# Optimization experiments

Measured on AMD Instinct MI355X. Metric: run time of the kernel, lower is better.

Reference implementation:

```python
import jax, jax.numpy as jnp
import numpy as np

N = 30000      # nodes
IN = 768       # input feature dim
C = 128        # hidden channels (= conv out_dim, = gate dim)
HEADS = 4      # attention heads (TransformerConv and Semantic)
DH = 128       # per-head dim (concat=False -> out_channels)
R = 3          # num relations
E = 80000      # edges per relation
NEG = 0.01     # LeakyReLU slope


def setup_inputs() -> dict:
    key = jax.random.key(0)
    ks = iter(jax.random.split(key, 64))
    def nx(shape):
        return jax.random.normal(next(ks), shape, dtype=jnp.float32) * 0.02
    inp = {}
    inp["x"] = jax.random.normal(next(ks), (N, IN), dtype=jnp.float32)
    inp["edges"] = jax.random.randint(next(ks), (R, 2, E), 0, N, dtype=jnp.int32)
    inp["lin1_W"] = nx((IN, C)); inp["lin1_b"] = jnp.zeros((C,), jnp.float32)
    for l in ("l1", "l2"):
        inp[f"{l}_Wq"] = nx((R, C, HEADS * DH)); inp[f"{l}_bq"] = jnp.zeros((R, HEADS * DH), jnp.float32)
        inp[f"{l}_Wk"] = nx((R, C, HEADS * DH)); inp[f"{l}_bk"] = jnp.zeros((R, HEADS * DH), jnp.float32)
        inp[f"{l}_Wv"] = nx((R, C, HEADS * DH)); inp[f"{l}_bv"] = jnp.zeros((R, HEADS * DH), jnp.float32)
        inp[f"{l}_Ws"] = nx((R, C, DH));         inp[f"{l}_bs"] = jnp.zeros((R, DH), jnp.float32)
        inp[f"{l}_gW"] = nx((C + DH, C));        inp[f"{l}_gb"] = jnp.zeros((C,), jnp.float32)
        inp[f"{l}_sW1"] = nx((HEADS, C, C));     inp[f"{l}_sb1"] = jnp.zeros((HEADS, C), jnp.float32)
        inp[f"{l}_sw2"] = nx((HEADS, C))
    inp["lin2_W"] = nx((C, C)); inp["lin2_b"] = jnp.zeros((C,), jnp.float32)
    inp["clf_W"] = nx((C, 2)); inp["clf_b"] = jnp.zeros((2,), jnp.float32)
    return inp


def lrelu(x):
    return jnp.where(x >= 0, x, NEG * x)


def transformer_conv(x, src, dst, Wq, bq, Wk, bk, Wv, bv, Ws, bs):
    # PyG TransformerConv, heads=HEADS, concat=False (head mean), root_weight=True, eval (no dropout)
    n = x.shape[0]
    q = (x @ Wq + bq).reshape(n, HEADS, DH)
    k = (x @ Wk + bk).reshape(n, HEADS, DH)
    v = (x @ Wv + bv).reshape(n, HEADS, DH)
    logits = (q[dst] * k[src]).sum(-1) / np.sqrt(DH)      # [E, H]
    m = jax.ops.segment_max(logits, dst, num_segments=n)  # scatter-softmax (stable)
    a = jnp.exp(logits - m[dst])
    s = jax.ops.segment_sum(a, dst, num_segments=n)
    alpha = a / s[dst]
    agg = jax.ops.segment_sum(alpha[:, :, None] * v[src], dst, num_segments=n)  # [N, H, DH]
    return agg.mean(axis=1) + x @ Ws + bs


def semantic(Hm, sW1, sb1, sw2):
    # Hm: [N, R, C]; per-head scoring MLP -> softmax over relations -> weighted sum, averaged over heads
    t = jnp.tanh(jnp.einsum('nrc,hco->hnro', Hm, sW1) + sb1[:, None, None, :])  # [H, N, R, C]
    scores = jnp.einsum('hnro,ho->hnr', t, sw2).mean(axis=1)                    # [H, R]
    beta = jax.nn.softmax(scores, axis=-1)
    return jnp.einsum('hr,nrc->nc', beta, Hm) / HEADS


def rgt_layer(x, edges, Wq, bq, Wk, bk, Wv, bv, Ws, bs, gW, gb, sW1, sb1, sw2):
    Hs = []
    for r in range(R):  # small fixed relation loop
        src, dst = edges[r, 0], edges[r, 1]
        U = transformer_conv(x, src, dst, Wq[r], bq[r], Wk[r], bk[r], Wv[r], bv[r], Ws[r], bs[r])
        Z = jax.nn.sigmoid(jnp.concatenate([U, x], axis=1) @ gW + gb)
        Hs.append(jnp.tanh(U) * Z + x * (1.0 - Z))
    Hm = jnp.stack(Hs, axis=1)  # [N, R, C]
    return semantic(Hm, sW1, sb1, sw2)


def reference(x, edges, lin1_W, lin1_b,
              l1_Wq, l1_bq, l1_Wk, l1_bk, l1_Wv, l1_bv, l1_Ws, l1_bs, l1_gW, l1_gb, l1_sW1, l1_sb1, l1_sw2,
              l2_Wq, l2_bq, l2_Wk, l2_bk, l2_Wv, l2_bv, l2_Ws, l2_bs, l2_gW, l2_gb, l2_sW1, l2_sb1, l2_sw2,
              lin2_W, lin2_b, clf_W, clf_b):
    h = lrelu(x @ lin1_W + lin1_b)
    h = rgt_layer(h, edges, l1_Wq, l1_bq, l1_Wk, l1_bk, l1_Wv, l1_bv, l1_Ws, l1_bs, l1_gW, l1_gb, l1_sW1, l1_sb1, l1_sw2)
    h = rgt_layer(h, edges, l2_Wq, l2_bq, l2_Wk, l2_bk, l2_Wv, l2_bv, l2_Ws, l2_bs, l2_gW, l2_gb, l2_sW1, l2_sb1, l2_sw2)
    h = lrelu(h @ lin2_W + lin2_b)
    return h @ clf_W + clf_b
```

## Files before the change

kernel.cpp:

```cpp
#include <hip/hip_runtime.h>
#include <math.h>

#define Nn 30000
#define RR 3
#define EE 80000
#define MT_M 235

#define SAP 72
#define EP_LD 68
#define KBIG 0x40000000

typedef __attribute__((ext_vector_type(8))) short bf16x8;
typedef __attribute__((ext_vector_type(4))) float f32x4;

__device__ __forceinline__ unsigned short f2bf(float f) {
    union { float f; unsigned u; } v; v.f = f;
    unsigned r = v.u + 0x7fff + ((v.u >> 16) & 1);
    return (unsigned short)(r >> 16);
}
__device__ __forceinline__ float fast_tanh(float x) {
    float e = __expf(2.f * x);
    return 1.f - 2.f / (e + 1.f);
}
__device__ __forceinline__ void unpack8(uint4 u, float* f) {
    union { unsigned u; float f; } a;
    a.u = u.x << 16;          f[0] = a.f;
    a.u = u.x & 0xffff0000u;  f[1] = a.f;
    a.u = u.y << 16;          f[2] = a.f;
    a.u = u.y & 0xffff0000u;  f[3] = a.f;
    a.u = u.z << 16;          f[4] = a.f;
    a.u = u.z & 0xffff0000u;  f[5] = a.f;
    a.u = u.w << 16;          f[6] = a.f;
    a.u = u.w & 0xffff0000u;  f[7] = a.f;
}

__device__ __forceinline__ void mfma_core(
    const short* __restrict__ A, int lda,
    const short* __restrict__ A2, int lda2, int ksplit,
    const short* __restrict__ Bt,
    int M, int K, int m0, int n0,
    short* As, short* Bs, f32x4 (&acc)[4][4])
{
    const int t = threadIdx.x;
    const int srow = t >> 3;
    const int scol = (t & 7) << 3;
    const int lane = t & 63;
    const int wave = t >> 6;
    const int wm = (wave >> 1) << 6;
    const int wn = (wave & 1) << 6;
    const int fr = lane & 15;
    const int quad = lane >> 4;
// ... 70 lines not shown
                ws[(quad * 4 + reg) * EP_LD + ni * 16 + fr] = acc[mi][ni][reg];
        int gr = m0 + wm + mi * 16 + rrow;
        if (gr >= M) continue;
        int gc = n0 + wn + cseg;
        float vals[16];
        #pragma unroll
        for (int j = 0; j < 16; j++) {
            float v = ws[rrow * EP_LD + cseg + j] + bias[gc + j];
            if (act == 1) v = (v >= 0.f) ? v : 0.01f * v;
            vals[j] = v;
        }
        if (C) {
            float* cp = C + (size_t)gr * ldc + gc;
            #pragma unroll
            for (int j4 = 0; j4 < 4; j4++)
                *(float4*)(cp + j4 * 4) = make_float4(vals[j4 * 4], vals[j4 * 4 + 1],
                                                      vals[j4 * 4 + 2], vals[j4 * 4 + 3]);
        }
        if (Cbf) {
            unsigned pk[8];
            #pragma unroll
            for (int j2 = 0; j2 < 8; j2++)
                pk[j2] = ((unsigned)f2bf(vals[2 * j2 + 1]) << 16) | (unsigned)f2bf(vals[2 * j2]);
            unsigned* bp = (unsigned*)(Cbf + (size_t)gr * ldcbf + gc);
            *(uint4*)bp       = make_uint4(pk[0], pk[1], pk[2], pk[3]);
            *(uint4*)(bp + 4) = make_uint4(pk[4], pk[5], pk[6], pk[7]);
        }
    }
}

__global__ __launch_bounds__(256) void gemm_qkvs_v4(
    const short* __restrict__ A,
    const short* __restrict__ Wt, const float* __restrict__ bias,
    short* __restrict__ qhat3, short* __restrict__ Ubf, int M)
{
    __shared__ short As[128 * SAP];
    __shared__ short Bs[128 * SAP];
    f32x4 acc[4][4];
    #pragma unroll
    for (int i = 0; i < 4; i++)
        #pragma unroll
        for (int j = 0; j < 4; j++) acc[i][j] = (f32x4){0.f, 0.f, 0.f, 0.f};
    int m0 = blockIdx.y * 128, bx = blockIdx.x, n0 = bx * 128;
    mfma_core(A, 128, A, 128, KBIG, Wt, M, 128, m0, n0, As, Bs, acc);

    const int t = threadIdx.x;
    const int lane = t & 63, wave = t >> 6;
    const int wm = (wave >> 1) << 6, wn = (wave & 1) << 6;
    const int fr = lane & 15, quad = lane >> 4;
    float* ws = (float*)As + wave * 16 * EP_LD;
    const int rrow = lane >> 2;
    const int cseg = (lane & 3) << 4;
    #pragma unroll
    for (int mi = 0; mi < 4; mi++) {
        #pragma unroll
        for (int ni = 0; ni < 4; ni++)
            #pragma unroll
            for (int reg = 0; reg < 4; reg++)
                ws[(quad * 4 + reg) * EP_LD + ni * 16 + fr] = acc[mi][ni][reg];
        int gr = m0 + wm + mi * 16 + rrow;
        if (gr >= M) continue;
        int lc = wn + cseg;
        float vals[16];
        #pragma unroll
        for (int j = 0; j < 16; j++)
            vals[j] = ws[rrow * EP_LD + cseg + j] + bias[n0 + lc + j];
        unsigned pk[8];
        #pragma unroll
        for (int j2 = 0; j2 < 8; j2++)
            pk[j2] = ((unsigned)f2bf(vals[2 * j2 + 1]) << 16) | (unsigned)f2bf(vals[2 * j2]);
        short* dst;
        if (bx < 12) {
            int r = bx >> 2;
            dst = qhat3 + ((size_t)(r * Nn + gr)) * 512 + (bx - r * 4) * 128 + lc;
        } else {
            dst = Ubf + (size_t)gr * 384 + (bx - 12) * 128 + lc;
        }
        unsigned* bp = (unsigned*)dst;
        *(uint4*)bp       = make_uint4(pk[0], pk[1], pk[2], pk[3]);
        *(uint4*)(bp + 4) = make_uint4(pk[4], pk[5], pk[6], pk[7]);
    }
}

__global__ __launch_bounds__(256) void attn_v4(
    const short* __restrict__ qhat3, const short* __restrict__ hbf,
    const int* __restrict__ rowptr3, const int* __restrict__ col3,
    short* __restrict__ Ah3)
{
    int wid = ((blockIdx.x * blockDim.x + threadIdx.x) >> 6);
    int lane = threadIdx.x & 63;
    if (wid >= 3 * Nn) return;
    int r = wid / Nn, n = wid - r * Nn;
    const int* rowptr = rowptr3 + r * (Nn + 1);
    const int* colb = col3 + r * EE;
    int beg = rowptr[n], end = rowptr[n + 1];

    uint4 qv = ((const uint4*)(qhat3 + ((size_t)r * Nn + n) * 512))[lane];
    float qf[8];
    unpack8(qv, qf);
    const int l16 = lane & 15;

    float m = -INFINITY, s = 0.f;
    float acc[8] = {0.f, 0.f, 0.f, 0.f, 0.f, 0.f, 0.f, 0.f};

    for (int i = beg; i < end; i++) {
        int src = colb[i];
        uint4 hv = ((const uint4*)(hbf + (size_t)src * 128))[l16];
        float hf[8];
        unpack8(hv, hf);
        float p = qf[0] * hf[0] + qf[1] * hf[1] + qf[2] * hf[2] + qf[3] * hf[3]
                + qf[4] * hf[4] + qf[5] * hf[5] + qf[6] * hf[6] + qf[7] * hf[7];
        p += __shfl_xor(p, 1);
        p += __shfl_xor(p, 2);
        p += __shfl_xor(p, 4);
        p += __shfl_xor(p, 8);
        float nm = fmaxf(m, p);
        float sc = __expf(m - nm);
        float pe = __expf(p - nm);
        s = s * sc + pe;
        #pragma unroll
        for (int j = 0; j < 8; j++) acc[j] = acc[j] * sc + pe * hf[j];
        m = nm;
    }

    float inv = (s > 0.f) ? 1.f / s : 0.f;
    #pragma unroll
    for (int j = 0; j < 8; j++) acc[j] *= inv;

    unsigned p0 = ((unsigned)f2bf(acc[1]) << 16) | (unsigned)f2bf(acc[0]);
    unsigned p1 = ((unsigned)f2bf(acc[3]) << 16) | (unsigned)f2bf(acc[2]);
    unsigned p2 = ((unsigned)f2bf(acc[5]) << 16) | (unsigned)f2bf(acc[4]);
    unsigned p3 = ((unsigned)f2bf(acc[7]) << 16) | (unsigned)f2bf(acc[6]);
    *(uint4*)(Ah3 + ((size_t)r * Nn + n) * 512 + lane * 8) = make_uint4(p0, p1, p2, p3);
}

__global__ __launch_bounds__(256) void ufin_mfma(
    const short* __restrict__ Ah3, const short* __restrict__ wvst,
    const float* __restrict__ bvmean, const int* __restrict__ rowptr3,
    short* __restrict__ U_bf, int M)
{
    __shared__ short As[128 * SAP];
    __shared__ short Bs[128 * SAP];
    f32x4 acc[4][4];
    #pragma unroll
    for (int i = 0; i < 4; i++)
        #pragma unroll
        for (int j = 0; j < 4; j++) acc[i][j] = (f32x4){0.f, 0.f, 0.f, 0.f};
    int r = blockIdx.z;
    int m0 = blockIdx.y * 128;
    const short* Ar = Ah3 + (size_t)r * Nn * 512;
    mfma_core(Ar, 512, Ar, 512, KBIG, wvst + r * 65536, M, 512, m0, 0, As, Bs, acc);

    const int t = threadIdx.x;
    const int lane = t & 63, wave = t >> 6;
    const int wm = (wave >> 1) << 6, wn = (wave & 1) << 6;
    const int fr = lane & 15, quad = lane >> 4;
    float* ws = (float*)As + wave * 16 * EP_LD;
    const int rrow = lane >> 2;
    const int cseg = (lane & 3) << 4;
    #pragma unroll
    for (int mi = 0; mi < 4; mi++) {
        #pragma unroll
        for (int ni = 0; ni < 4; ni++)
            #pragma unroll
            for (int reg = 0; reg < 4; reg++)
                ws[(quad * 4 + reg) * EP_LD + ni * 16 + fr] = acc[mi][ni][reg];
        int gr = m0 + wm + mi * 16 + rrow;
        if (gr >= M) continue;
        int gc = wn + cseg;
        int be = rowptr3[r * (Nn + 1) + gr];
        int en = rowptr3[r * (Nn + 1) + gr + 1];
        float mk = (en > be) ? 1.f : 0.f;
        short* up = U_bf + (size_t)gr * 384 + r * 128 + gc;
        uint4 u0 = *(const uint4*)up;
        uint4 u1 = *(const uint4*)(up + 8);
        float uv[16];
        unpack8(u0, uv); unpack8(u1, uv + 8);
        float vals[16];
        #pragma unroll
        for (int j = 0; j < 16; j++)
            vals[j] = ws[rrow * EP_LD + cseg + j] + uv[j] + mk * bvmean[r * 128 + gc + j];
        unsigned pk[8];
        #pragma unroll
        for (int j2 = 0; j2 < 8; j2++)
            pk[j2] = ((unsigned)f2bf(vals[2 * j2 + 1]) << 16) | (unsigned)f2bf(vals[2 * j2]);
        unsigned* bp = (unsigned*)up;
        *(uint4*)bp       = make_uint4(pk[0], pk[1], pk[2], pk[3]);
        *(uint4*)(bp + 4) = make_uint4(pk[4], pk[5], pk[6], pk[7]);
    }
}

__global__ __launch_bounds__(256) void gate_mfma(
    const short* __restrict__ Ubf,
    const short* __restrict__ Hbf,
    const short* __restrict__ gWt, const float* __restrict__ gb,
    const float* __restrict__ Hf,
    float* __restrict__ Hm, short* __restrict__ HmBf,
    int M)
{
    __shared__ short As[128 * SAP];
    __shared__ short Bs[128 * SAP];
    f32x4 acc[4][4];
    #pragma unroll
    for (int i = 0; i < 4; i++)
        #pragma unroll
        for (int j = 0; j < 4; j++) acc[i][j] = (f32x4){0.f, 0.f, 0.f, 0.f};
    int r = blockIdx.z;
    int m0 = blockIdx.y * 128;
    mfma_core(Ubf + r * 128, 384, Hbf, 128, 128, gWt, M, 256, m0, 0, As, Bs, acc);

    const int t = threadIdx.x;
    const int lane = t & 63, wave = t >> 6;
    const int wm = (wave >> 1) << 6, wn = (wave & 1) << 6;
    const int fr = lane & 15, quad = lane >> 4;
    float* ws = (float*)As + wave * 16 * EP_LD;
    const int rrow = lane >> 2;
    const int cseg = (lane & 3) << 4;
    #pragma unroll
    for (int mi = 0; mi < 4; mi++) {
        #pragma unroll
        for (int ni = 0; ni < 4; ni++)
            #pragma unroll
            for (int reg = 0; reg < 4; reg++)
                ws[(quad * 4 + reg) * EP_LD + ni * 16 + fr] = acc[mi][ni][reg];
        int gr = m0 + wm + mi * 16 + rrow;
        if (gr >= M) continue;
        int gc = wn + cseg;
        const short* up = Ubf + (size_t)gr * 384 + r * 128 + gc;
        const float* hp = Hf + (size_t)gr * 128 + gc;
        float uv[16], hv[16];
        uint4 u0 = *(const uint4*)up;
        uint4 u1 = *(const uint4*)(up + 8);
        unpack8(u0, uv); unpack8(u1, uv + 8);
        #pragma unroll
        for (int j4 = 0; j4 < 4; j4++)
            *(float4*)(hv + j4 * 4) = *(const float4*)(hp + j4 * 4);
        float vals[16];
        #pragma unroll
        for (int j = 0; j < 16; j++) {
            float g = ws[rrow * EP_LD + cseg + j] + gb[gc + j];
            float z = 1.f / (1.f + __expf(-g));
            vals[j] = fast_tanh(uv[j]) * z + hv[j] * (1.f - z);
        }
        float* cp = Hm + (size_t)gr * 384 + r * 128 + gc;
        #pragma unroll
        for (int j4 = 0; j4 < 4; j4++)
            *(float4*)(cp + j4 * 4) = make_float4(vals[j4 * 4], vals[j4 * 4 + 1],
                                                  vals[j4 * 4 + 2], vals[j4 * 4 + 3]);
        unsigned pk[8];
        #pragma unroll
        for (int j2 = 0; j2 < 8; j2++)
            pk[j2] = ((unsigned)f2bf(vals[2 * j2 + 1]) << 16) | (unsigned)f2bf(vals[2 * j2]);
        unsigned* bp = (unsigned*)(HmBf + (size_t)gr * 384 + r * 128 + gc);
        *(uint4*)bp       = make_uint4(pk[0], pk[1], pk[2], pk[3]);
        *(uint4*)(bp + 4) = make_uint4(pk[4], pk[5], pk[6], pk[7]);
    }
}

__global__ __launch_bounds__(256) void semantic_mfma(
    const short* __restrict__ HmBf, const short* __restrict__ sW1t,
    const float* __restrict__ sb1, const float* __restrict__ sw2,
    float* __restrict__ partial, int M)
{
    __shared__ short As[128 * SAP];
    __shared__ short Bs[128 * SAP];
    __shared__ float red4[4];
    f32x4 acc[4][4];
    #pragma unroll
    for (int i = 0; i < 4; i++)
        #pragma unroll
        for (int j = 0; j < 4; j++) acc[i][j] = (f32x4){0.f, 0.f, 0.f, 0.f};
    int head = blockIdx.x, r = blockIdx.z;
    int m0 = blockIdx.y * 128, n0 = head * 128;
    mfma_core(HmBf + r * 128, 384, HmBf + r * 128, 384, KBIG, sW1t, M, 128, m0, n0, As, Bs, acc);
    const int t = threadIdx.x;
    const int lane = t & 63, wave = t >> 6;
    const int wm = (wave >> 1) << 6, wn = (wave & 1) << 6;
    const int fr = lane & 15, quad = lane >> 4;
    float local = 0.f;
    #pragma unroll
    for (int ni = 0; ni < 4; ni++) {
        int gc = n0 + wn + ni * 16 + fr;
        float b = sb1[gc], w2 = sw2[gc];
        #pragma unroll
        for (int mi = 0; mi < 4; mi++) {
            #pragma unroll
            for (int reg = 0; reg < 4; reg++) {
                int gr = m0 + wm + mi * 16 + quad * 4 + reg;
// ... 53 lines not shown
    float w0 = w[0], w1 = w[1], w2 = w[2];
    float4 v = make_float4(w0 * a.x + w1 * b.x + w2 * c.x,
                           w0 * a.y + w1 * b.y + w2 * c.y,
                           w0 * a.z + w1 * b.z + w2 * c.z,
                           w0 * a.w + w1 * b.w + w2 * c.w);
    *(float4*)(h + (size_t)n * 128 + c4) = v;
    unsigned p0 = ((unsigned)f2bf(v.y) << 16) | (unsigned)f2bf(v.x);
    unsigned p1 = ((unsigned)f2bf(v.w) << 16) | (unsigned)f2bf(v.z);
    *(uint2*)(hbf + (size_t)n * 128 + c4) = make_uint2(p0, p1);
}

__global__ void convert_bf16_kernel(const float* __restrict__ src, unsigned* __restrict__ dst, int n_pairs)
{
    int i = blockIdx.x * blockDim.x + threadIdx.x;
    if (i >= n_pairs) return;
    float2 f = ((const float2*)src)[i];
    dst[i] = ((unsigned)f2bf(f.y) << 16) | (unsigned)f2bf(f.x);
}

__global__ void prep_global_kernel(const float* __restrict__ lin1_W, const float* __restrict__ lin2_W,
                                   short* __restrict__ lin1Wt, short* __restrict__ lin2Wt)
{
    int id = blockIdx.x * blockDim.x + threadIdx.x;
    if (id < 98304) {
        int n = id / 768, k = id % 768;
        lin1Wt[id] = (short)f2bf(lin1_W[k * 128 + n]);
    } else if (id < 114688) {
        int r = id - 98304;
        int n = r / 128, k = r % 128;
        lin2Wt[r] = (short)f2bf(lin2_W[k * 128 + n]);
    }
}

__global__ void prep_layer_v4(
    const float* __restrict__ Ws, const float* __restrict__ bs,
    const float* __restrict__ gW, const float* __restrict__ sW1,
    const float* __restrict__ Wv, const float* __restrict__ bv,
    short* __restrict__ Wt4, short* __restrict__ gWt,
    short* __restrict__ sW1t, short* __restrict__ wvst,
    float* __restrict__ B4, float* __restrict__ bvmean)
{
    const int S0 = 49152;
    const int S1 = S0 + 32768;
    const int S2 = S1 + 65536;
    const int S3 = S2 + 196608;
    const int S4 = S3 + 384;
    const int S5 = S4 + 384;
    int id = blockIdx.x * blockDim.x + threadIdx.x;
    if (id < S0) {
        int n = id / 128, k = id - n * 128;
        int r = n >> 7, c = n & 127;
        Wt4[(size_t)(1536 + n) * 128 + k] = (short)f2bf(Ws[(size_t)r * 16384 + k * 128 + c]);
    } else if (id < S1) {
        int q = id - S0;
        int n = q / 256, k = q - n * 256;
        gWt[q] = (short)f2bf(gW[k * 128 + n]);
    } else if (id < S2) {
        int q = id - S1;
        int h = q / 16384, rem = q - h * 16384;
        int n = rem / 128, k = rem - n * 128;
        sW1t[q] = (short)f2bf(sW1[(size_t)h * 16384 + k * 128 + n]);
    } else if (id < S3) {
        int q = id - S2;
        int r = q / 65536, rem = q - r * 65536;
        int d = rem / 512, mcol = rem - d * 512;
        int hh = mcol >> 7, j = mcol & 127;
        wvst[q] = (short)f2bf(0.25f * Wv[(size_t)r * 65536 + j * 512 + hh * 128 + d]);
    } else if (id < S4) {
        int q = id - S3;
        B4[1536 + q] = bs[q];
    } else if (id < S5) {
        int q = id - S4;
        int r = q >> 7, d = q & 127;
        bvmean[q] = 0.25f * (bv[r * 512 + d] + bv[r * 512 + 128 + d]
                           + bv[r * 512 + 256 + d] + bv[r * 512 + 384 + d]);
    }
}

__global__ __launch_bounds__(256) void gmat_v2(
    const float* __restrict__ Wq0, const float* __restrict__ Wk0, const float* __restrict__ bq0,
    const float* __restrict__ Wq1, const float* __restrict__ Wk1, const float* __restrict__ bq1,
    short* __restrict__ Wt4, float* __restrict__ B4)
{
    __shared__ float WqL[128 * 129];
    __shared__ float WkL[16 * 128];
    const int jg = blockIdx.x;
    const int h  = blockIdx.y;
    const int lz = blockIdx.z;
    const int l = lz / 3, r = lz - l * 3;
    const float* Wq = l ? Wq1 : Wq0;
    const float* Wk = l ? Wk1 : Wk0;
    const float* bq = l ? bq1 : bq0;
    short* Wt = Wt4 + (size_t)l * 245760;
    float* Bb = B4 + l * 1920;
    const float scale = 0.088388347648318447f;
    const int t = threadIdx.x;

    for (int v = t; v < 4096; v += 256) {
        int i = v >> 5, d4 = (v & 31) << 2;
        float4 q = *(const float4*)(Wq + (size_t)r * 65536 + i * 512 + h * 128 + d4);
        float* wp = WqL + i * 129 + d4;
        wp[0] = q.x; wp[1] = q.y; wp[2] = q.z; wp[3] = q.w;
    }
    for (int v = t; v < 512; v += 256) {
        int jl = v >> 5, d4 = (v & 31) << 2;
        float4 q = *(const float4*)(Wk + (size_t)r * 65536 + (jg * 16 + jl) * 512 + h * 128 + d4);
        float* wp = WkL + jl * 128 + d4;
        wp[0] = q.x; wp[1] = q.y; wp[2] = q.z; wp[3] = q.w;
    }
    __syncthreads();

    const int i = t & 127;
    const int jh = t >> 7;
    const float* wk = WkL + jh * 8 * 128;
    float acc[8] = {0.f, 0.f, 0.f, 0.f, 0.f, 0.f, 0.f, 0.f};
    #pragma unroll 4
    for (int d = 0; d < 128; d++) {
        float wq = WqL[i * 129 + d];
        #pragma unroll
        for (int jj = 0; jj < 8; jj++)
            acc[jj] += wq * wk[jj * 128 + d];
    }
    short* wrow = Wt + ((size_t)(r * 512 + h * 128 + jg * 16 + jh * 8)) * 128 + i;
    #pragma unroll
    for (int jj = 0; jj < 8; jj++)
        wrow[(size_t)jj * 128] = (short)f2bf(scale * acc[jj]);

// ... 71 lines not shown
    if (n >= M) return;
    const float* row = t + (size_t)n * 128;
    float a0 = b[0], a1 = b[1];
    #pragma unroll
    for (int kk = 0; kk < 128; kk++) {
        float a = row[kk];
        a0 += a * W[kk * 2];
        a1 += a * W[kk * 2 + 1];
    }
    out[n * 2] = a0;
    out[n * 2 + 1] = a1;
}

extern "C" void kernel_launch(void* const* d_in, const int* in_sizes, int n_in,
                              void* d_out, int out_size, void* d_ws, size_t ws_size,
                              hipStream_t stream)
{
    const float* x      = (const float*)d_in[0];
    const int*   edges  = (const int*)d_in[1];
    const float* lin1_W = (const float*)d_in[2];
    const float* lin1_b = (const float*)d_in[3];
    const int L0 = 4, L1 = 17;
    const float* lin2_W = (const float*)d_in[30];
    const float* lin2_b = (const float*)d_in[31];
    const float* clf_W  = (const float*)d_in[32];
    const float* clf_b  = (const float*)d_in[33];
    float* out = (float*)d_out;

    char* w = (char*)d_ws;
    size_t off = 0;
    auto alloc = [&](size_t bytes) { void* p = w + off; off = (off + bytes + 255) & ~(size_t)255; return p; };
    float* h      = (float*)alloc((size_t)Nn * 128 * 4);
    short* h_bf   = (short*)alloc((size_t)Nn * 128 * 2);
    short* U_bf   = (short*)alloc((size_t)Nn * 384 * 2);
    const size_t QH = (size_t)3 * Nn * 512 * 2;
    char* BIG     = (char*)alloc(2 * QH);
    short* qhat3  = (short*)BIG;
    short* Ah3    = (short*)(BIG + QH);
    short* x_bf   = (short*)BIG;
    float* Hm     = (float*)BIG;
    short* Hm_bf  = (short*)(BIG + (size_t)Nn * 384 * 4);
    float* lin2o  = (float*)BIG;
    short* lin1Wt = (short*)alloc((size_t)98304 * 2);
    short* lin2Wt = (short*)alloc((size_t)16384 * 2);
    short* qkvsWt4 = (short*)alloc((size_t)2 * 245760 * 2);
    short* gWt    = (short*)alloc((size_t)2 * 32768 * 2);
    short* sW1t   = (short*)alloc((size_t)2 * 65536 * 2);
    short* wvst   = (short*)alloc((size_t)2 * 196608 * 2);
    float* qkvsB4 = (float*)alloc((size_t)2 * 1920 * 4);
    float* bvmean = (float*)alloc((size_t)2 * 384 * 4);
    int* rowptr3  = (int*)alloc((size_t)3 * (Nn + 1) * 4);
    int* cnt3     = (int*)alloc((size_t)3 * Nn * 4);
    int* col3     = (int*)alloc((size_t)3 * EE * 4);
    float* partial = (float*)alloc((size_t)12 * MT_M * 4);
    float* scores = (float*)alloc(12 * 4);
    float* wmix   = (float*)alloc(3 * 4);

    const int MT = MT_M;
    dim3 blk(256);

    {
        int n_pairs = Nn * 768 / 2;
        convert_bf16_kernel<<<(n_pairs + 255) / 256, blk, 0, stream>>>(x, (unsigned*)x_bf, n_pairs);
        prep_global_kernel<<<(114688 + 255) / 256, blk, 0, stream>>>(lin1_W, lin2_W, lin1Wt, lin2Wt);
        for (int l = 0; l < 2; l++) {
            int base = (l == 0) ? L0 : L1;
            prep_layer_v4<<<(344832 + 255) / 256, blk, 0, stream>>>(
                (const float*)d_in[base + 6], (const float*)d_in[base + 7],
                (const float*)d_in[base + 8], (const float*)d_in[base + 10],
                (const float*)d_in[base + 4], (const float*)d_in[base + 5],
                qkvsWt4 + (size_t)l * 245760, gWt + (size_t)l * 32768,
                sW1t + (size_t)l * 65536, wvst + (size_t)l * 196608,
                qkvsB4 + (size_t)l * 1920, bvmean + (size_t)l * 384);
        }
        gmat_v2<<<dim3(8, 4, 6), blk, 0, stream>>>(
            (const float*)d_in[L0 + 0], (const float*)d_in[L0 + 2], (const float*)d_in[L0 + 1],
            (const float*)d_in[L1 + 0], (const float*)d_in[L1 + 2], (const float*)d_in[L1 + 1],
            qkvsWt4, qkvsB4);
        zero_i32_kernel<<<(3 * Nn + 255) / 256, blk, 0, stream>>>(cnt3, 3 * Nn);
        hist3_kernel<<<(3 * EE + 255) / 256, blk, 0, stream>>>(edges, cnt3);
        scan3_kernel<<<3, 1024, 0, stream>>>(cnt3, rowptr3);
        zero_i32_kernel<<<(3 * Nn + 255) / 256, blk, 0, stream>>>(cnt3, 3 * Nn);
        scatter3_kernel<<<(3 * EE + 255) / 256, blk, 0, stream>>>(edges, rowptr3, cnt3, col3);
    }

    gemm_mfma<<<dim3(1, MT), blk, 0, stream>>>(
        x_bf, 768, x_bf, 768, KBIG, lin1Wt, lin1_b, h, 128, h_bf, 128, Nn, 768, 1);

    for (int l = 0; l < 2; l++) {
        int base = (l == 0) ? L0 : L1;
        const float* gb  = (const float*)d_in[base + 9];
        const float* sb1 = (const float*)d_in[base + 11];
        const float* sw2 = (const float*)d_in[base + 12];
        short* lWt4   = qkvsWt4 + (size_t)l * 245760;
        short* lgWt   = gWt + (size_t)l * 32768;
        short* lsW1t  = sW1t + (size_t)l * 65536;
        short* lwvst  = wvst + (size_t)l * 196608;
        float* lB4    = qkvsB4 + (size_t)l * 1920;
        float* lbvm   = bvmean + (size_t)l * 384;

        gemm_qkvs_v4<<<dim3(15, MT), blk, 0, stream>>>(
            h_bf, lWt4, lB4, qhat3, U_bf, Nn);

        attn_v4<<<(3 * Nn + 3) / 4, blk, 0, stream>>>(qhat3, h_bf, rowptr3, col3, Ah3);

        ufin_mfma<<<dim3(1, MT, 3), blk, 0, stream>>>(Ah3, lwvst, lbvm, rowptr3, U_bf, Nn);

        gate_mfma<<<dim3(1, MT, 3), blk, 0, stream>>>(
            U_bf, h_bf, lgWt, gb, h, Hm, Hm_bf, Nn);

        semantic_mfma<<<dim3(4, MT, 3), blk, 0, stream>>>(Hm_bf, lsW1t, sb1, sw2, partial, Nn);
        reduce12_kernel<<<12, 64, 0, stream>>>(partial, scores);
        compute_w_kernel<<<1, 64, 0, stream>>>(scores, wmix, 1.f / (float)Nn);
        mix_kernel<<<(Nn * 32 + 255) / 256, blk, 0, stream>>>(Hm, wmix, h, h_bf, Nn * 32);
    }

    gemm_mfma<<<dim3(1, MT), blk, 0, stream>>>(
        h_bf, 128, h_bf, 128, KBIG, lin2Wt, lin2_b, lin2o, 128, (short*)nullptr, 0, Nn, 128, 1);
    clf_kernel<<<(Nn + 255) / 256, blk, 0, stream>>>(lin2o, clf_W, clf_b, out, Nn);
}
```

Measured before the change: 812.5 us.

## Fuse value projection, skip projection and gate into one MFMA kernel

The root/skip projection (h@Ws) moves out of the QKVS GEMM and into the value-projection GEMM by concatenating K to 640 (Ah3 plus h). The result U stays in LDS as bf16, and the gating GEMM plus sigmoid/tanh blend run in the same kernel. This removes the U_bf round-trip through global memory and one kernel launch per layer. In exchange, the gate GEMM reads B fragments straight from global without LDS staging, and the epilogue writes Hm with scalar per-element stores instead of vectorised ones.

```diff
diff --git a/kernel.cpp b/kernel.cpp
--- a/kernel.cpp
+++ b/kernel.cpp
@@ -8,6 +8,7 @@
 
 #define SAP 72
 #define EP_LD 68
+#define UTS 136
 #define KBIG 0x40000000
 
 typedef __attribute__((ext_vector_type(8))) short bf16x8;
@@ -17,6 +18,11 @@
     union { float f; unsigned u; } v; v.f = f;
     unsigned r = v.u + 0x7fff + ((v.u >> 16) & 1);
     return (unsigned short)(r >> 16);
+}
+__device__ __forceinline__ float bf2f(short h) {
+    union { unsigned u; float f; } v;
+    v.u = ((unsigned)(unsigned short)h) << 16;
+    return v.f;
 }
 __device__ __forceinline__ float fast_tanh(float x) {
     float e = __expf(2.f * x);
@@ -153,7 +159,7 @@
 __global__ __launch_bounds__(256) void gemm_qkvs_v4(
     const short* __restrict__ A,
     const short* __restrict__ Wt, const float* __restrict__ bias,
-    short* __restrict__ qhat3, short* __restrict__ Ubf, int M)
+    short* __restrict__ qhat3, int M)
 {
     __shared__ short As[128 * SAP];
     __shared__ short Bs[128 * SAP];
@@ -172,6 +178,7 @@
     float* ws = (float*)As + wave * 16 * EP_LD;
     const int rrow = lane >> 2;
     const int cseg = (lane & 3) << 4;
+    const int r = bx >> 2;
     #pragma unroll
     for (int mi = 0; mi < 4; mi++) {
         #pragma unroll
@@ -190,14 +197,7 @@
         #pragma unroll
         for (int j2 = 0; j2 < 8; j2++)
             pk[j2] = ((unsigned)f2bf(vals[2 * j2 + 1]) << 16) | (unsigned)f2bf(vals[2 * j2]);
-        short* dst;
-        if (bx < 12) {
-            int r = bx >> 2;
-            dst = qhat3 + ((size_t)(r * Nn + gr)) * 512 + (bx - r * 4) * 128 + lc;
-        } else {
-            dst = Ubf + (size_t)gr * 384 + (bx - 12) * 128 + lc;
-        }
-        unsigned* bp = (unsigned*)dst;
+        unsigned* bp = (unsigned*)(qhat3 + ((size_t)(r * Nn + gr)) * 512 + (bx - r * 4) * 128 + lc);
         *(uint4*)bp       = make_uint4(pk[0], pk[1], pk[2], pk[3]);
         *(uint4*)(bp + 4) = make_uint4(pk[4], pk[5], pk[6], pk[7]);
     }
@@ -255,126 +255,102 @@
     *(uint4*)(Ah3 + ((size_t)r * Nn + n) * 512 + lane * 8) = make_uint4(p0, p1, p2, p3);
 }
 
-__global__ __launch_bounds__(256) void ufin_mfma(
-    const short* __restrict__ Ah3, const short* __restrict__ wvst,
-    const float* __restrict__ bvmean, const int* __restrict__ rowptr3,
-    short* __restrict__ U_bf, int M)
-{
-    __shared__ short As[128 * SAP];
-    __shared__ short Bs[128 * SAP];
+__global__ __launch_bounds__(256) void ugate_mfma(
+    const short* __restrict__ Ah3, const short* __restrict__ w640t,
+    const float* __restrict__ bs, const float* __restrict__ bvmean,
+    const int* __restrict__ rowptr3,
+    const short* __restrict__ gWt, const float* __restrict__ gb,
+    const short* __restrict__ Hbf, const float* __restrict__ Hf,
+    float* __restrict__ Hm, short* __restrict__ HmBf, int M)
+{
+    __shared__ short LDSb[2 * 128 * SAP];
+    short* As = LDSb;
+    short* Bs = LDSb + 128 * SAP;
     f32x4 acc[4][4];
     #pragma unroll
     for (int i = 0; i < 4; i++)
         #pragma unroll
         for (int j = 0; j < 4; j++) acc[i][j] = (f32x4){0.f, 0.f, 0.f, 0.f};
-    int r = blockIdx.z;
-    int m0 = blockIdx.y * 128;
-    const short* Ar = Ah3 + (size_t)r * Nn * 512;
-    mfma_core(Ar, 512, Ar, 512, KBIG, wvst + r * 65536, M, 512, m0, 0, As, Bs, acc);
+    const int r = blockIdx.z;
+    const int m0 = blockIdx.y * 128;
+    mfma_core(Ah3 + (size_t)r * Nn * 512, 512, Hbf, 128, 512,
+              w640t + (size_t)r * 81920, M, 640, m0, 0, As, Bs, acc);
 
     const int t = threadIdx.x;
     const int lane = t & 63, wave = t >> 6;
     const int wm = (wave >> 1) << 6, wn = (wave & 1) << 6;
     const int fr = lane & 15, quad = lane >> 4;
-    float* ws = (float*)As + wave * 16 * EP_LD;
-    const int rrow = lane >> 2;
-    const int cseg = (lane & 3) << 4;
+    short* Ut = LDSb;
+    const int rp = r * (Nn + 1);
+
     #pragma unroll
     for (int mi = 0; mi < 4; mi++) {
         #pragma unroll
+        for (int reg = 0; reg < 4; reg++) {
+            int row = wm + mi * 16 + quad * 4 + reg;
+            int gr = m0 + row;
+            float mk = 0.f;
+            if (gr < M) mk = (rowptr3[rp + gr + 1] > rowptr3[rp + gr]) ? 1.f : 0.f;
+            #pragma unroll
+            for (int ni = 0; ni < 4; ni++) {
+                int col = wn + ni * 16 + fr;
+                float u = acc[mi][ni][reg] + bs[r * 128 + col] + mk * bvmean[r * 128 + col];
+                Ut[row * UTS + col] = (short)f2bf(u);
+            }
+        }
+    }
+    __syncthreads();
+
+    f32x4 gacc[4][4];
+    #pragma unroll
+    for (int i = 0; i < 4; i++)
+        #pragma unroll
+        for (int j = 0; j < 4; j++) gacc[i][j] = (f32x4){0.f, 0.f, 0.f, 0.f};
+    #pragma unroll
+    for (int kc = 0; kc < 8; kc++) {
+        bf16x8 af[4], bfr[4];
+        #pragma unroll
+        for (int mi = 0; mi < 4; mi++) {
+            int row = wm + mi * 16 + fr;
+            if (kc < 4) {
+                af[mi] = *(const bf16x8*)(Ut + row * UTS + kc * 32 + quad * 8);
+            } else {
+                int gr = m0 + row;
+                bf16x8 v = {0, 0, 0, 0, 0, 0, 0, 0};
+                if (gr < M) v = *(const bf16x8*)(Hbf + (size_t)gr * 128 + (kc - 4) * 32 + quad * 8);
+                af[mi] = v;
+            }
+        }
+        #pragma unroll
         for (int ni = 0; ni < 4; ni++)
-            #pragma unroll
-            for (int reg = 0; reg < 4; reg++)
-                ws[(quad * 4 + reg) * EP_LD + ni * 16 + fr] = acc[mi][ni][reg];
-        int gr = m0 + wm + mi * 16 + rrow;
-        if (gr >= M) continue;
-        int gc = wn + cseg;
-        int be = rowptr3[r * (Nn + 1) + gr];
-        int en = rowptr3[r * (Nn + 1) + gr + 1];
-        float mk = (en > be) ? 1.f : 0.f;
-        short* up = U_bf + (size_t)gr * 384 + r * 128 + gc;
-        uint4 u0 = *(const uint4*)up;
-        uint4 u1 = *(const uint4*)(up + 8);
-        float uv[16];
-        unpack8(u0, uv); unpack8(u1, uv + 8);
-        float vals[16];
-        #pragma unroll
-        for (int j = 0; j < 16; j++)
-            vals[j] = ws[rrow * EP_LD + cseg + j] + uv[j] + mk * bvmean[r * 128 + gc + j];
-        unsigned pk[8];
-        #pragma unroll
-        for (int j2 = 0; j2 < 8; j2++)
-            pk[j2] = ((unsigned)f2bf(vals[2 * j2 + 1]) << 16) | (unsigned)f2bf(vals[2 * j2]);
-        unsigned* bp = (unsigned*)up;
-        *(uint4*)bp       = make_uint4(pk[0], pk[1], pk[2], pk[3]);
-        *(uint4*)(bp + 4) = make_uint4(pk[4], pk[5], pk[6], pk[7]);
-    }
-}
-
-__global__ __launch_bounds__(256) void gate_mfma(
-    const short* __restrict__ Ubf,
-    const short* __restrict__ Hbf,
-    const short* __restrict__ gWt, const float* __restrict__ gb,
-    const float* __restrict__ Hf,
-    float* __restrict__ Hm, short* __restrict__ HmBf,
-    int M)
-{
-    __shared__ short As[128 * SAP];
-    __shared__ short Bs[128 * SAP];
-    f32x4 acc[4][4];
-    #pragma unroll
-    for (int i = 0; i < 4; i++)
-        #pragma unroll
-        for (int j = 0; j < 4; j++) acc[i][j] = (f32x4){0.f, 0.f, 0.f, 0.f};
-    int r = blockIdx.z;
-    int m0 = blockIdx.y * 128;
-    mfma_core(Ubf + r * 128, 384, Hbf, 128, 128, gWt, M, 256, m0, 0, As, Bs, acc);
-
-    const int t = threadIdx.x;
-    const int lane = t & 63, wave = t >> 6;
-    const int wm = (wave >> 1) << 6, wn = (wave & 1) << 6;
-    const int fr = lane & 15, quad = lane >> 4;
-    float* ws = (float*)As + wave * 16 * EP_LD;
-    const int rrow = lane >> 2;
-    const int cseg = (lane & 3) << 4;
+            bfr[ni] = *(const bf16x8*)(gWt + (size_t)(wn + ni * 16 + fr) * 256 + kc * 32 + quad * 8);
+        #pragma unroll
+        for (int mi = 0; mi < 4; mi++)
+            #pragma unroll
+            for (int ni = 0; ni < 4; ni++)
+                gacc[mi][ni] = __builtin_amdgcn_mfma_f32_16x16x32_bf16(
+                    af[mi], bfr[ni], gacc[mi][ni], 0, 0, 0);
+    }
+
     #pragma unroll
     for (int mi = 0; mi < 4; mi++) {
         #pragma unroll
-        for (int ni = 0; ni < 4; ni++)
-            #pragma unroll
-            for (int reg = 0; reg < 4; reg++)
-                ws[(quad * 4 + reg) * EP_LD + ni * 16 + fr] = acc[mi][ni][reg];
-        int gr = m0 + wm + mi * 16 + rrow;
-        if (gr >= M) continue;
-        int gc = wn + cseg;
-        const short* up = Ubf + (size_t)gr * 384 + r * 128 + gc;
-        const float* hp = Hf + (size_t)gr * 128 + gc;
-        float uv[16], hv[16];
-        uint4 u0 = *(const uint4*)up;
-        uint4 u1 = *(const uint4*)(up + 8);
-        unpack8(u0, uv); unpack8(u1, uv + 8);
-        #pragma unroll
-        for (int j4 = 0; j4 < 4; j4++)
-            *(float4*)(hv + j4 * 4) = *(const float4*)(hp + j4 * 4);
-        float vals[16];
-        #pragma unroll
-        for (int j = 0; j < 16; j++) {
-            float g = ws[rrow * EP_LD + cseg + j] + gb[gc + j];
-            float z = 1.f / (1.f + __expf(-g));
-            vals[j] = fast_tanh(uv[j]) * z + hv[j] * (1.f - z);
-        }
-        float* cp = Hm + (size_t)gr * 384 + r * 128 + gc;
-        #pragma unroll
-        for (int j4 = 0; j4 < 4; j4++)
-            *(float4*)(cp + j4 * 4) = make_float4(vals[j4 * 4], vals[j4 * 4 + 1],
-                                                  vals[j4 * 4 + 2], vals[j4 * 4 + 3]);
-        unsigned pk[8];
-        #pragma unroll
-        for (int j2 = 0; j2 < 8; j2++)
-            pk[j2] = ((unsigned)f2bf(vals[2 * j2 + 1]) << 16) | (unsigned)f2bf(vals[2 * j2]);
-        unsigned* bp = (unsigned*)(HmBf + (size_t)gr * 384 + r * 128 + gc);
-        *(uint4*)bp       = make_uint4(pk[0], pk[1], pk[2], pk[3]);
-        *(uint4*)(bp + 4) = make_uint4(pk[4], pk[5], pk[6], pk[7]);
+        for (int reg = 0; reg < 4; reg++) {
+            int row = wm + mi * 16 + quad * 4 + reg;
+            int gr = m0 + row;
+            if (gr >= M) continue;
+            #pragma unroll
+            for (int ni = 0; ni < 4; ni++) {
+                int gc = wn + ni * 16 + fr;
+                float g = gacc[mi][ni][reg] + gb[gc];
+                float z = 1.f / (1.f + __expf(-g));
+                float uvv = bf2f(Ut[row * UTS + gc]);
+                float hvv = Hf[(size_t)gr * 128 + gc];
+                float val = fast_tanh(uvv) * z + hvv * (1.f - z);
+                Hm[(size_t)gr * 384 + r * 128 + gc] = val;
+                HmBf[(size_t)gr * 384 + r * 128 + gc] = (short)f2bf(val);
+            }
+        }
     }
 }
 
@@ -494,45 +470,40 @@
     }
 }
 
-__global__ void prep_layer_v4(
-    const float* __restrict__ Ws, const float* __restrict__ bs,
-    const float* __restrict__ gW, const float* __restrict__ sW1,
-    const float* __restrict__ Wv, const float* __restrict__ bv,
-    short* __restrict__ Wt4, short* __restrict__ gWt,
-    short* __restrict__ sW1t, short* __restrict__ wvst,
-    float* __restrict__ B4, float* __restrict__ bvmean)
-{
-    const int S0 = 49152;
-    const int S1 = S0 + 32768;
-    const int S2 = S1 + 65536;
-    const int S3 = S2 + 196608;
-    const int S4 = S3 + 384;
-    const int S5 = S4 + 384;
+__global__ void prep_layer_v6(
+    const float* __restrict__ Ws, const float* __restrict__ gW,
+    const float* __restrict__ sW1, const float* __restrict__ Wv,
+    const float* __restrict__ bv,
+    short* __restrict__ gWt, short* __restrict__ sW1t,
+    short* __restrict__ w640t, float* __restrict__ bvmean)
+{
+    const int S0 = 32768;
+    const int S1 = S0 + 65536;
+    const int S2 = S1 + 245760;
+    const int S3 = S2 + 384;
     int id = blockIdx.x * blockDim.x + threadIdx.x;
     if (id < S0) {
-        int n = id / 128, k = id - n * 128;
-        int r = n >> 7, c = n & 127;
-        Wt4[(size_t)(1536 + n) * 128 + k] = (short)f2bf(Ws[(size_t)r * 16384 + k * 128 + c]);
+        int n = id / 256, k = id - n * 256;
+        gWt[id] = (short)f2bf(gW[k * 128 + n]);
     } else if (id < S1) {
         int q = id - S0;
-        int n = q / 256, k = q - n * 256;
-        gWt[q] = (short)f2bf(gW[k * 128 + n]);
-    } else if (id < S2) {
-        int q = id - S1;
         int h = q / 16384, rem = q - h * 16384;
         int n = rem / 128, k = rem - n * 128;
         sW1t[q] = (short)f2bf(sW1[(size_t)h * 16384 + k * 128 + n]);
+    } else if (id < S2) {
+        int q = id - S1;
+        int r = q / 81920, rem = q - r * 81920;
+        int d = rem / 640, k = rem - d * 640;
+        float v;
+        if (k < 512) {
+            int hh = k >> 7, j = k & 127;
+            v = 0.25f * Wv[(size_t)r * 65536 + j * 512 + hh * 128 + d];
+        } else {
+            v = Ws[(size_t)r * 16384 + (k - 512) * 128 + d];
+        }
+        w640t[q] = (short)f2bf(v);
     } else if (id < S3) {
         int q = id - S2;
-        int r = q / 65536, rem = q - r * 65536;
-        int d = rem / 512, mcol = rem - d * 512;
-        int hh = mcol >> 7, j = mcol & 127;
-        wvst[q] = (short)f2bf(0.25f * Wv[(size_t)r * 65536 + j * 512 + hh * 128 + d]);
-    } else if (id < S4) {
-        int q = id - S3;
-        B4[1536 + q] = bs[q];
-    } else if (id < S5) {
-        int q = id - S4;
         int r = q >> 7, d = q & 127;
         bvmean[q] = 0.25f * (bv[r * 512 + d] + bv[r * 512 + 128 + d]
                            + bv[r * 512 + 256 + d] + bv[r * 512 + 384 + d]);
@@ -553,8 +524,8 @@
     const float* Wq = l ? Wq1 : Wq0;
     const float* Wk = l ? Wk1 : Wk0;
     const float* bq = l ? bq1 : bq0;
-    short* Wt = Wt4 + (size_t)l * 245760;
-    float* Bb = B4 + l * 1920;
+    short* Wt = Wt4 + (size_t)l * 196608;
+    float* Bb = B4 + l * 1536;
     const float scale = 0.088388347648318447f;
     const int t = threadIdx.x;
 
@@ -692,7 +663,6 @@
     auto alloc = [&](size_t bytes) { void* p = w + off; off = (off + bytes + 255) & ~(size_t)255; return p; };
     float* h      = (float*)alloc((size_t)Nn * 128 * 4);
     short* h_bf   = (short*)alloc((size_t)Nn * 128 * 2);
-    short* U_bf   = (short*)alloc((size_t)Nn * 384 * 2);
     const size_t QH = (size_t)3 * Nn * 512 * 2;
     char* BIG     = (char*)alloc(2 * QH);
     short* qhat3  = (short*)BIG;
@@ -703,11 +673,11 @@
     float* lin2o  = (float*)BIG;
     short* lin1Wt = (short*)alloc((size_t)98304 * 2);
     short* lin2Wt = (short*)alloc((size_t)16384 * 2);
-    short* qkvsWt4 = (short*)alloc((size_t)2 * 245760 * 2);
+    short* qkvsWt4 = (short*)alloc((size_t)2 * 196608 * 2);
     short* gWt    = (short*)alloc((size_t)2 * 32768 * 2);
     short* sW1t   = (short*)alloc((size_t)2 * 65536 * 2);
-    short* wvst   = (short*)alloc((size_t)2 * 196608 * 2);
-    float* qkvsB4 = (float*)alloc((size_t)2 * 1920 * 4);
+    short* w640t  = (short*)alloc((size_t)2 * 245760 * 2);
+    float* qkvsB4 = (float*)alloc((size_t)2 * 1536 * 4);
     float* bvmean = (float*)alloc((size_t)2 * 384 * 4);
     int* rowptr3  = (int*)alloc((size_t)3 * (Nn + 1) * 4);
     int* cnt3     = (int*)alloc((size_t)3 * Nn * 4);
@@ -725,13 +695,12 @@
         prep_global_kernel<<<(114688 + 255) / 256, blk, 0, stream>>>(lin1_W, lin2_W, lin1Wt, lin2Wt);
         for (int l = 0; l < 2; l++) {
             int base = (l == 0) ? L0 : L1;
-            prep_layer_v4<<<(344832 + 255) / 256, blk, 0, stream>>>(
-                (const float*)d_in[base + 6], (const float*)d_in[base + 7],
-                (const float*)d_in[base + 8], (const float*)d_in[base + 10],
-                (const float*)d_in[base + 4], (const float*)d_in[base + 5],
-                qkvsWt4 + (size_t)l * 245760, gWt + (size_t)l * 32768,
-                sW1t + (size_t)l * 65536, wvst + (size_t)l * 196608,
-                qkvsB4 + (size_t)l * 1920, bvmean + (size_t)l * 384);
+            prep_layer_v6<<<(344448 + 255) / 256, blk, 0, stream>>>(
+                (const float*)d_in[base + 6], (const float*)d_in[base + 8],
+                (const float*)d_in[base + 10], (const float*)d_in[base + 4],
+                (const float*)d_in[base + 5],
+                gWt + (size_t)l * 32768, sW1t + (size_t)l * 65536,
+                w640t + (size_t)l * 245760, bvmean + (size_t)l * 384);
         }
         gmat_v2<<<dim3(8, 4, 6), blk, 0, stream>>>(
             (const float*)d_in[L0 + 0], (const float*)d_in[L0 + 2], (const float*)d_in[L0 + 1],
@@ -749,25 +718,24 @@
 
     for (int l = 0; l < 2; l++) {
         int base = (l == 0) ? L0 : L1;
+        const float* bs  = (const float*)d_in[base + 7];
         const float* gb  = (const float*)d_in[base + 9];
         const float* sb1 = (const float*)d_in[base + 11];
         const float* sw2 = (const float*)d_in[base + 12];
-        short* lWt4   = qkvsWt4 + (size_t)l * 245760;
+        short* lWt4   = qkvsWt4 + (size_t)l * 196608;
         short* lgWt   = gWt + (size_t)l * 32768;
         short* lsW1t  = sW1t + (size_t)l * 65536;
-        short* lwvst  = wvst + (size_t)l * 196608;
-        float* lB4    = qkvsB4 + (size_t)l * 1920;
+        short* lw640  = w640t + (size_t)l * 245760;
+        float* lB4    = qkvsB4 + (size_t)l * 1536;
         float* lbvm   = bvmean + (size_t)l * 384;
 
-        gemm_qkvs_v4<<<dim3(15, MT), blk, 0, stream>>>(
-            h_bf, lWt4, lB4, qhat3, U_bf, Nn);
+        gemm_qkvs_v4<<<dim3(12, MT), blk, 0, stream>>>(
+            h_bf, lWt4, lB4, qhat3, Nn);
 
         attn_v4<<<(3 * Nn + 3) / 4, blk, 0, stream>>>(qhat3, h_bf, rowptr3, col3, Ah3);
 
-        ufin_mfma<<<dim3(1, MT, 3), blk, 0, stream>>>(Ah3, lwvst, lbvm, rowptr3, U_bf, Nn);
-
-        gate_mfma<<<dim3(1, MT, 3), blk, 0, stream>>>(
-            U_bf, h_bf, lgWt, gb, h, Hm, Hm_bf, Nn);
+        ugate_mfma<<<dim3(1, MT, 3), blk, 0, stream>>>(
+            Ah3, lw640, bs, lbvm, rowptr3, lgWt, gb, h_bf, h, Hm, Hm_bf, Nn);
 
         semantic_mfma<<<dim3(4, MT, 3), blk, 0, stream>>>(Hm_bf, lsW1t, sb1, sw2, partial, Nn);
         reduce12_kernel<<<12, 64, 0, stream>>>(partial, scores);
```

After: 830.2 us. 1.02x slower.

## Fuse root-weight projection into ufin GEMM and prefetch neighbor rows in attention

Applied to the files above, without the earlier changes.

The skip/root projection (x@Ws+bs) moves out of the QKVS GEMM, which drops from 15 to 12 column blocks, and into the ufin MFMA GEMM by concatenating h_bf onto the Ah3 operand, giving a K=640 GEMM. This removes the U_bf write in the QKVS kernel and its read-back in the ufin epilogue. The attention loop also software-prefetches the next neighbor's feature row to hide gather latency. The cost is a longer K loop in ufin and a relaid-out weight prep.

```diff
diff --git a/kernel.cpp b/kernel.cpp
--- a/kernel.cpp
+++ b/kernel.cpp
@@ -17,6 +17,11 @@
     union { float f; unsigned u; } v; v.f = f;
     unsigned r = v.u + 0x7fff + ((v.u >> 16) & 1);
     return (unsigned short)(r >> 16);
+}
+__device__ __forceinline__ float bf2f(short h) {
+    union { unsigned u; float f; } v;
+    v.u = ((unsigned)(unsigned short)h) << 16;
+    return v.f;
 }
 __device__ __forceinline__ float fast_tanh(float x) {
     float e = __expf(2.f * x);
@@ -153,7 +158,7 @@
 __global__ __launch_bounds__(256) void gemm_qkvs_v4(
     const short* __restrict__ A,
     const short* __restrict__ Wt, const float* __restrict__ bias,
-    short* __restrict__ qhat3, short* __restrict__ Ubf, int M)
+    short* __restrict__ qhat3, int M)
 {
     __shared__ short As[128 * SAP];
     __shared__ short Bs[128 * SAP];
@@ -172,6 +177,7 @@
     float* ws = (float*)As + wave * 16 * EP_LD;
     const int rrow = lane >> 2;
     const int cseg = (lane & 3) << 4;
+    const int r = bx >> 2;
     #pragma unroll
     for (int mi = 0; mi < 4; mi++) {
         #pragma unroll
@@ -190,14 +196,7 @@
         #pragma unroll
         for (int j2 = 0; j2 < 8; j2++)
             pk[j2] = ((unsigned)f2bf(vals[2 * j2 + 1]) << 16) | (unsigned)f2bf(vals[2 * j2]);
-        short* dst;
-        if (bx < 12) {
-            int r = bx >> 2;
-            dst = qhat3 + ((size_t)(r * Nn + gr)) * 512 + (bx - r * 4) * 128 + lc;
-        } else {
-            dst = Ubf + (size_t)gr * 384 + (bx - 12) * 128 + lc;
-        }
-        unsigned* bp = (unsigned*)dst;
+        unsigned* bp = (unsigned*)(qhat3 + ((size_t)(r * Nn + gr)) * 512 + (bx - r * 4) * 128 + lc);
         *(uint4*)bp       = make_uint4(pk[0], pk[1], pk[2], pk[3]);
         *(uint4*)(bp + 4) = make_uint4(pk[4], pk[5], pk[6], pk[7]);
     }
@@ -224,9 +223,13 @@
     float m = -INFINITY, s = 0.f;
     float acc[8] = {0.f, 0.f, 0.f, 0.f, 0.f, 0.f, 0.f, 0.f};
 
+    uint4 hv_n = make_uint4(0, 0, 0, 0);
+    if (beg < end)
+        hv_n = ((const uint4*)(hbf + (size_t)colb[beg] * 128))[l16];
     for (int i = beg; i < end; i++) {
-        int src = colb[i];
-        uint4 hv = ((const uint4*)(hbf + (size_t)src * 128))[l16];
+        uint4 hv = hv_n;
+        if (i + 1 < end)
+            hv_n = ((const uint4*)(hbf + (size_t)colb[i + 1] * 128))[l16];
         float hf[8];
         unpack8(hv, hf);
         float p = qf[0] * hf[0] + qf[1] * hf[1] + qf[2] * hf[2] + qf[3] * hf[3]
@@ -256,8 +259,10 @@
 }
 
 __global__ __launch_bounds__(256) void ufin_mfma(
-    const short* __restrict__ Ah3, const short* __restrict__ wvst,
-    const float* __restrict__ bvmean, const int* __restrict__ rowptr3,
+    const short* __restrict__ Ah3, const short* __restrict__ Hbf,
+    const short* __restrict__ w640t,
+    const float* __restrict__ bs, const float* __restrict__ bvmean,
+    const int* __restrict__ rowptr3,
     short* __restrict__ U_bf, int M)
 {
     __shared__ short As[128 * SAP];
@@ -269,8 +274,8 @@
         for (int j = 0; j < 4; j++) acc[i][j] = (f32x4){0.f, 0.f, 0.f, 0.f};
     int r = blockIdx.z;
     int m0 = blockIdx.y * 128;
-    const short* Ar = Ah3 + (size_t)r * Nn * 512;
-    mfma_core(Ar, 512, Ar, 512, KBIG, wvst + r * 65536, M, 512, m0, 0, As, Bs, acc);
+    mfma_core(Ah3 + (size_t)r * Nn * 512, 512, Hbf, 128, 512,
+              w640t + (size_t)r * 81920, M, 640, m0, 0, As, Bs, acc);
 
     const int t = threadIdx.x;
     const int lane = t & 63, wave = t >> 6;
@@ -279,6 +284,7 @@
     float* ws = (float*)As + wave * 16 * EP_LD;
     const int rrow = lane >> 2;
     const int cseg = (lane & 3) << 4;
+    const int rp = r * (Nn + 1);
     #pragma unroll
     for (int mi = 0; mi < 4; mi++) {
         #pragma unroll
@@ -289,23 +295,17 @@
         int gr = m0 + wm + mi * 16 + rrow;
         if (gr >= M) continue;
         int gc = wn + cseg;
-        int be = rowptr3[r * (Nn + 1) + gr];
-        int en = rowptr3[r * (Nn + 1) + gr + 1];
-        float mk = (en > be) ? 1.f : 0.f;
-        short* up = U_bf + (size_t)gr * 384 + r * 128 + gc;
-        uint4 u0 = *(const uint4*)up;
-        uint4 u1 = *(const uint4*)(up + 8);
-        float uv[16];
-        unpack8(u0, uv); unpack8(u1, uv + 8);
+        float mk = (rowptr3[rp + gr + 1] > rowptr3[rp + gr]) ? 1.f : 0.f;
         float vals[16];
         #pragma unroll
         for (int j = 0; j < 16; j++)
-            vals[j] = ws[rrow * EP_LD + cseg + j] + uv[j] + mk * bvmean[r * 128 + gc + j];
+            vals[j] = ws[rrow * EP_LD + cseg + j] + bs[r * 128 + gc + j]
+                    + mk * bvmean[r * 128 + gc + j];
         unsigned pk[8];
         #pragma unroll
         for (int j2 = 0; j2 < 8; j2++)
             pk[j2] = ((unsigned)f2bf(vals[2 * j2 + 1]) << 16) | (unsigned)f2bf(vals[2 * j2]);
-        unsigned* bp = (unsigned*)up;
+        unsigned* bp = (unsigned*)(U_bf + (size_t)gr * 384 + r * 128 + gc);
         *(uint4*)bp       = make_uint4(pk[0], pk[1], pk[2], pk[3]);
         *(uint4*)(bp + 4) = make_uint4(pk[4], pk[5], pk[6], pk[7]);
     }
@@ -494,45 +494,40 @@
     }
 }
 
-__global__ void prep_layer_v4(
-    const float* __restrict__ Ws, const float* __restrict__ bs,
-    const float* __restrict__ gW, const float* __restrict__ sW1,
-    const float* __restrict__ Wv, const float* __restrict__ bv,
-    short* __restrict__ Wt4, short* __restrict__ gWt,
-    short* __restrict__ sW1t, short* __restrict__ wvst,
-    float* __restrict__ B4, float* __restrict__ bvmean)
-{
-    const int S0 = 49152;
-    const int S1 = S0 + 32768;
-    const int S2 = S1 + 65536;
-    const int S3 = S2 + 196608;
-    const int S4 = S3 + 384;
-    const int S5 = S4 + 384;
+__global__ void prep_layer_v6(
+    const float* __restrict__ Ws, const float* __restrict__ gW,
+    const float* __restrict__ sW1, const float* __restrict__ Wv,
+    const float* __restrict__ bv,
+    short* __restrict__ gWt, short* __restrict__ sW1t,
+    short* __restrict__ w640t, float* __restrict__ bvmean)
+{
+    const int S0 = 32768;
+    const int S1 = S0 + 65536;
+    const int S2 = S1 + 245760;
+    const int S3 = S2 + 384;
     int id = blockIdx.x * blockDim.x + threadIdx.x;
     if (id < S0) {
-        int n = id / 128, k = id - n * 128;
-        int r = n >> 7, c = n & 127;
-        Wt4[(size_t)(1536 + n) * 128 + k] = (short)f2bf(Ws[(size_t)r * 16384 + k * 128 + c]);
+        int n = id / 256, k = id - n * 256;
+        gWt[id] = (short)f2bf(gW[k * 128 + n]);
     } else if (id < S1) {
         int q = id - S0;
-        int n = q / 256, k = q - n * 256;
-        gWt[q] = (short)f2bf(gW[k * 128 + n]);
-    } else if (id < S2) {
-        int q = id - S1;
         int h = q / 16384, rem = q - h * 16384;
         int n = rem / 128, k = rem - n * 128;
         sW1t[q] = (short)f2bf(sW1[(size_t)h * 16384 + k * 128 + n]);
+    } else if (id < S2) {
+        int q = id - S1;
+        int r = q / 81920, rem = q - r * 81920;
+        int d = rem / 640, k = rem - d * 640;
+        float v;
+        if (k < 512) {
+            int hh = k >> 7, j = k & 127;
+            v = 0.25f * Wv[(size_t)r * 65536 + j * 512 + hh * 128 + d];
+        } else {
+            v = Ws[(size_t)r * 16384 + (k - 512) * 128 + d];
+        }
+        w640t[q] = (short)f2bf(v);
     } else if (id < S3) {
         int q = id - S2;
-        int r = q / 65536, rem = q - r * 65536;
-        int d = rem / 512, mcol = rem - d * 512;
-        int hh = mcol >> 7, j = mcol & 127;
-        wvst[q] = (short)f2bf(0.25f * Wv[(size_t)r * 65536 + j * 512 + hh * 128 + d]);
-    } else if (id < S4) {
-        int q = id - S3;
-        B4[1536 + q] = bs[q];
-    } else if (id < S5) {
-        int q = id - S4;
         int r = q >> 7, d = q & 127;
         bvmean[q] = 0.25f * (bv[r * 512 + d] + bv[r * 512 + 128 + d]
                            + bv[r * 512 + 256 + d] + bv[r * 512 + 384 + d]);
@@ -553,8 +548,8 @@
     const float* Wq = l ? Wq1 : Wq0;
     const float* Wk = l ? Wk1 : Wk0;
     const float* bq = l ? bq1 : bq0;
-    short* Wt = Wt4 + (size_t)l * 245760;
-    float* Bb = B4 + l * 1920;
+    short* Wt = Wt4 + (size_t)l * 196608;
+    float* Bb = B4 + l * 1536;
     const float scale = 0.088388347648318447f;
     const int t = threadIdx.x;
 
@@ -703,11 +698,11 @@
     float* lin2o  = (float*)BIG;
     short* lin1Wt = (short*)alloc((size_t)98304 * 2);
     short* lin2Wt = (short*)alloc((size_t)16384 * 2);
-    short* qkvsWt4 = (short*)alloc((size_t)2 * 245760 * 2);
+    short* qkvsWt4 = (short*)alloc((size_t)2 * 196608 * 2);
     short* gWt    = (short*)alloc((size_t)2 * 32768 * 2);
     short* sW1t   = (short*)alloc((size_t)2 * 65536 * 2);
-    short* wvst   = (short*)alloc((size_t)2 * 196608 * 2);
-    float* qkvsB4 = (float*)alloc((size_t)2 * 1920 * 4);
+    short* w640t  = (short*)alloc((size_t)2 * 245760 * 2);
+    float* qkvsB4 = (float*)alloc((size_t)2 * 1536 * 4);
     float* bvmean = (float*)alloc((size_t)2 * 384 * 4);
     int* rowptr3  = (int*)alloc((size_t)3 * (Nn + 1) * 4);
     int* cnt3     = (int*)alloc((size_t)3 * Nn * 4);
@@ -725,13 +720,12 @@
         prep_global_kernel<<<(114688 + 255) / 256, blk, 0, stream>>>(lin1_W, lin2_W, lin1Wt, lin2Wt);
         for (int l = 0; l < 2; l++) {
             int base = (l == 0) ? L0 : L1;
-            prep_layer_v4<<<(344832 + 255) / 256, blk, 0, stream>>>(
-                (const float*)d_in[base + 6], (const float*)d_in[base + 7],
-                (const float*)d_in[base + 8], (const float*)d_in[base + 10],
-                (const float*)d_in[base + 4], (const float*)d_in[base + 5],
-                qkvsWt4 + (size_t)l * 245760, gWt + (size_t)l * 32768,
-                sW1t + (size_t)l * 65536, wvst + (size_t)l * 196608,
-                qkvsB4 + (size_t)l * 1920, bvmean + (size_t)l * 384);
+            prep_layer_v6<<<(344448 + 255) / 256, blk, 0, stream>>>(
+                (const float*)d_in[base + 6], (const float*)d_in[base + 8],
+                (const float*)d_in[base + 10], (const float*)d_in[base + 4],
+                (const float*)d_in[base + 5],
+                gWt + (size_t)l * 32768, sW1t + (size_t)l * 65536,
+                w640t + (size_t)l * 245760, bvmean + (size_t)l * 384);
         }
         gmat_v2<<<dim3(8, 4, 6), blk, 0, stream>>>(
             (const float*)d_in[L0 + 0], (const float*)d_in[L0 + 2], (const float*)d_in[L0 + 1],
@@ -749,22 +743,24 @@
 
     for (int l = 0; l < 2; l++) {
         int base = (l == 0) ? L0 : L1;
+        const float* bs  = (const float*)d_in[base + 7];
         const float* gb  = (const float*)d_in[base + 9];
         const float* sb1 = (const float*)d_in[base + 11];
         const float* sw2 = (const float*)d_in[base + 12];
-        short* lWt4   = qkvsWt4 + (size_t)l * 245760;
+        short* lWt4   = qkvsWt4 + (size_t)l * 196608;
         short* lgWt   = gWt + (size_t)l * 32768;
         short* lsW1t  = sW1t + (size_t)l * 65536;
-        short* lwvst  = wvst + (size_t)l * 196608;
-        float* lB4    = qkvsB4 + (size_t)l * 1920;
+        short* lw640  = w640t + (size_t)l * 245760;
+        float* lB4    = qkvsB4 + (size_t)l * 1536;
         float* lbvm   = bvmean + (size_t)l * 384;
 
-        gemm_qkvs_v4<<<dim3(15, MT), blk, 0, stream>>>(
-            h_bf, lWt4, lB4, qhat3, U_bf, Nn);
+        gemm_qkvs_v4<<<dim3(12, MT), blk, 0, stream>>>(
+            h_bf, lWt4, lB4, qhat3, Nn);
 
         attn_v4<<<(3 * Nn + 3) / 4, blk, 0, stream>>>(qhat3, h_bf, rowptr3, col3, Ah3);
 
-        ufin_mfma<<<dim3(1, MT, 3), blk, 0, stream>>>(Ah3, lwvst, lbvm, rowptr3, U_bf, Nn);
+        ufin_mfma<<<dim3(1, MT, 3), blk, 0, stream>>>(
+            Ah3, h_bf, lw640, bs, lbvm, rowptr3, U_bf, Nn);
 
         gate_mfma<<<dim3(1, MT, 3), blk, 0, stream>>>(
             U_bf, h_bf, lgWt, gb, h, Hm, Hm_bf, Nn);
```

New measurement: 791.8 us. 2.6% less time.
